# Performance work log

Hardware: AMD Instinct MI355X
Metric: run time of the kernel (lower is better)

Reference implementation:

```python
import jax, jax.numpy as jnp
import numpy as np

B, N, C = 8, 1024, 768
H = 12
D = C // H  # head_dim = 64
SCALE = D ** -0.5
EPS = 1e-5


def _layer_norm(x):
    # per-head LayerNorm over last dim, gamma=1, beta=0, biased variance
    mean = x.mean(-1, keepdims=True)
    var = ((x - mean) ** 2).mean(-1, keepdims=True)
    return (x - mean) / jnp.sqrt(var + EPS)


def setup_inputs() -> dict:
    key = jax.random.key(0)
    k1, k2, k3 = jax.random.split(key, 3)
    x = jax.random.normal(k1, (B, N, C), dtype=jnp.float32)
    qkv_weight = jax.random.normal(k2, (3 * C, C), dtype=jnp.float32) * (C ** -0.5)
    proj_weight = jax.random.normal(k3, (C, C), dtype=jnp.float32) * (C ** -0.5)
    return {"x": x, "qkv_weight": qkv_weight, "proj_weight": proj_weight}


def reference(x, qkv_weight, proj_weight):
    Bx, Nx, Cx = x.shape
    qkv = x @ qkv_weight.T                          # [B,N,3C]
    qkv = qkv.reshape(Bx, Nx, 3, H, D).transpose(2, 0, 3, 1, 4)  # [3,B,H,N,D]
    q, k, v = qkv[0], qkv[1], qkv[2]
    q = _layer_norm(q) * SCALE
    k = _layer_norm(k)
    attn = jnp.einsum('bhnd,bhmd->bhnm', q, k)      # [B,H,N,N]
    attn = jax.nn.softmax(attn, axis=-1)
    out = jnp.einsum('bhnm,bhmd->bhnd', attn, v)    # [B,H,N,D]
    out = out.transpose(0, 2, 1, 3).reshape(Bx, Nx, Cx)
    return out @ proj_weight.T
```

## Files before the change

kernel.cpp:

```cpp
#include <hip/hip_runtime.h>
#include <stdint.h>
#include <stddef.h>

#define HB 8
#define HN 1024
#define HC 768
#define HH 12
#define HD 64
#define ROWS (HB*HN)
#define BH (HB*HH)

using s16x4  = __attribute__((ext_vector_type(4))) short;
using bf16x8 = __attribute__((ext_vector_type(8))) short;
using f32x4  = __attribute__((ext_vector_type(4))) float;

__device__ __forceinline__ short f2bf(float f) {
  union { float f; uint32_t u; } c; c.f = f;
  uint32_t u = c.u;
  uint32_t r = (u + 0x7fffu + ((u >> 16) & 1u)) >> 16;
  return (short)r;
}
__device__ __forceinline__ float bf2f(short s) {
  union { uint32_t u; float f; } c; c.u = ((uint32_t)(uint16_t)s) << 16;
  return c.f;
}
__device__ __forceinline__ uint32_t pack_bf16_rne(float a, float b) {
  union { float f; uint32_t u; } ca, cb; ca.f = a; cb.f = b;
  uint32_t ra = ca.u + 0x7fffu + ((ca.u >> 16) & 1u);
  uint32_t rb = cb.u + 0x7fffu + ((cb.u >> 16) & 1u);
  return __builtin_amdgcn_perm(rb, ra, 0x07060302);
}
__device__ __forceinline__ float fast_exp2(float x) {
#if __has_builtin(__builtin_amdgcn_exp2f)
  return __builtin_amdgcn_exp2f(x);
#else
  return exp2f(x);
#endif
}
__device__ __forceinline__ f32x4 mfma16(bf16x8 a, bf16x8 b, f32x4 c) {
  return __builtin_amdgcn_mfma_f32_16x16x32_bf16(a, b, c, 0, 0, 0);
}
__device__ __forceinline__ void gll16(const void* g, void* l) {
  __builtin_amdgcn_global_load_lds((const __attribute__((address_space(1))) void*)g,
                                   (__attribute__((address_space(3))) void*)l,
                                   16, 0, 0);
}

__global__ void cvt3_kernel(const float* __restrict__ x,  short* __restrict__ xb,  int n0,
                            const float* __restrict__ wq, short* __restrict__ wqb, int n1,
                            const float* __restrict__ wp, short* __restrict__ wpb, int n2) {
  int i = blockIdx.x * 256 + threadIdx.x;
  const float* in; short* out;
  if (i < n0)            { in = x;  out = xb;  }
  else if (i < n0 + n1)  { i -= n0; in = wq; out = wqb; }
  else if (i < n0 + n1 + n2) { i -= n0 + n1; in = wp; out = wpb; }
  else return;
  float4 v = ((const float4*)in)[i];
  s16x4 o;
  o.x = f2bf(v.x); o.y = f2bf(v.y); o.z = f2bf(v.z); o.w = f2bf(v.w);
  ((s16x4*)out)[i] = o;
}

__device__ __forceinline__ void store_c(float* p, float v) { *p = v; }
__device__ __forceinline__ void store_c(short* p, float v) { *p = f2bf(v); }

__global__ __launch_bounds__(256) void gemm_qkv(const short* __restrict__ A,
                                                const short* __restrict__ Bw,
                                                short* __restrict__ Qb,
                                                short* __restrict__ Kb,
                                                short* __restrict__ vb) {
  const int K = HC;
  __shared__ short As[128*64];
  __shared__ short Bs[128*64];
  const int m0 = blockIdx.y * 128, n0 = blockIdx.x * 128;
  const int tid = threadIdx.x;
  const int lane = tid & 63, w = tid >> 6, quad = lane >> 4, lc = lane & 15;
  const int wr = w >> 1, wc = w & 1;
  f32x4 acc[4][4] = {};
  for (int kt = 0; kt < K; kt += 64) {
#pragma unroll
    for (int i = 0; i < 4; ++i) {
      const int chunk = i*256 + tid;
      const int r = chunk >> 3, cb = chunk & 7;
      const int cbs = cb ^ (r & 7);
      gll16(A  + (size_t)(m0 + r)*K + kt + cbs*8, (void*)(As + (size_t)chunk*8));
      gll16(Bw + (size_t)(n0 + r)*K + kt + cbs*8, (void*)(Bs + (size_t)chunk*8));
    }
    __syncthreads();
#pragma unroll
    for (int kk = 0; kk < 2; ++kk) {
      bf16x8 af[4], bfr[4];
      const int kb = kk*4 + quad;
#pragma unroll
      for (int mt = 0; mt < 4; ++mt)
        af[mt] = *(const bf16x8*)(As + (wr*64 + mt*16 + lc)*64 + (kb ^ (lc & 7))*8);
#pragma unroll
      for (int nt = 0; nt < 4; ++nt)
        bfr[nt] = *(const bf16x8*)(Bs + (wc*64 + nt*16 + lc)*64 + (kb ^ (lc & 7))*8);
#pragma unroll
      for (int mt = 0; mt < 4; ++mt)
#pragma unroll
        for (int nt = 0; nt < 4; ++nt)
          acc[mt][nt] = mfma16(af[mt], bfr[nt], acc[mt][nt]);
    }
    __syncthreads();
  }
  const int cg = n0 + wc*64;
  const int t = cg / HC;
  const int h = (cg % HC) / HD;
  const int b = m0 >> 10;
  const int bh = b*HH + h;
  if (t < 2) {
    short* outp = (t == 0) ? Qb : Kb;
    const float sc = (t == 0) ? 0.125f : 1.0f;
#pragma unroll
    for (int mt = 0; mt < 4; ++mt)
#pragma unroll
      for (int r = 0; r < 4; ++r) {
        float s1 = (acc[mt][0][r] + acc[mt][1][r]) + (acc[mt][2][r] + acc[mt][3][r]);
        float s2 = acc[mt][0][r]*acc[mt][0][r];
        s2 = __builtin_fmaf(acc[mt][1][r], acc[mt][1][r], s2);
        s2 = __builtin_fmaf(acc[mt][2][r], acc[mt][2][r], s2);
        s2 = __builtin_fmaf(acc[mt][3][r], acc[mt][3][r], s2);
#pragma unroll
        for (int off = 1; off < 16; off <<= 1) {
          s1 += __shfl_xor(s1, off);
          s2 += __shfl_xor(s2, off);
        }
        const float mean = s1 * (1.0f/64.0f);
        const float var  = s2 * (1.0f/64.0f) - mean*mean;
        const float inv  = rsqrtf(var + 1e-5f) * sc;
        const int n_in = (m0 & 1023) + wr*64 + mt*16 + quad*4 + r;
        short* rowp = outp + ((size_t)bh*HN + n_in)*HD;
#pragma unroll
        for (int nt = 0; nt < 4; ++nt)
          rowp[nt*16 + lc] = f2bf((acc[mt][nt][r] - mean) * inv);
      }
  } else {
#pragma unroll
    for (int mt = 0; mt < 4; ++mt)
#pragma unroll
      for (int nt = 0; nt < 4; ++nt)
#pragma unroll
        for (int r = 0; r < 4; ++r) {
          const int row = m0 + wr*64 + mt*16 + quad*4 + r;
          const int col = h*HD + nt*16 + lc;
          vb[(size_t)row*HC + col] = f2bf(acc[mt][nt][r]);
        }
  }
}

__global__ __launch_bounds__(256) void gemm_bt_f32(const short* __restrict__ A,
                                                   const short* __restrict__ Bw,
                                                   float* __restrict__ C,
                                                   int M, int N, int K) {
  __shared__ short As[128*64];
  __shared__ short Bs[128*64];
  const int m0 = blockIdx.y * 128, n0 = blockIdx.x * 128;
  const int tid = threadIdx.x;
  const int lane = tid & 63, w = tid >> 6, quad = lane >> 4, lc = lane & 15;
  const int wr = w >> 1, wc = w & 1;
  f32x4 acc[4][4] = {};
  for (int kt = 0; kt < K; kt += 64) {
#pragma unroll
    for (int i = 0; i < 4; ++i) {
      const int chunk = i*256 + tid;
      const int r = chunk >> 3, cb = chunk & 7;
      const int cbs = cb ^ (r & 7);
      gll16(A  + (size_t)(m0 + r)*K + kt + cbs*8, (void*)(As + (size_t)chunk*8));
      gll16(Bw + (size_t)(n0 + r)*K + kt + cbs*8, (void*)(Bs + (size_t)chunk*8));
    }
    __syncthreads();
#pragma unroll
    for (int kk = 0; kk < 2; ++kk) {
      bf16x8 af[4], bfr[4];
      const int kb = kk*4 + quad;
#pragma unroll
      for (int mt = 0; mt < 4; ++mt)
        af[mt] = *(const bf16x8*)(As + (wr*64 + mt*16 + lc)*64 + (kb ^ (lc & 7))*8);
#pragma unroll
      for (int nt = 0; nt < 4; ++nt)
        bfr[nt] = *(const bf16x8*)(Bs + (wc*64 + nt*16 + lc)*64 + (kb ^ (lc & 7))*8);
#pragma unroll
      for (int mt = 0; mt < 4; ++mt)
#pragma unroll
        for (int nt = 0; nt < 4; ++nt)
          acc[mt][nt] = mfma16(af[mt], bfr[nt], acc[mt][nt]);
    }
    __syncthreads();
  }
#pragma unroll
  for (int mt = 0; mt < 4; ++mt)
#pragma unroll
    for (int nt = 0; nt < 4; ++nt)
#pragma unroll
      for (int r = 0; r < 4; ++r) {
        const int row = m0 + wr*64 + mt*16 + quad*4 + r;
        const int col = n0 + wc*64 + nt*16 + lc;
        store_c(C + (size_t)row*N + col, acc[mt][nt][r]);
      }
}

__global__ __launch_bounds__(256) void vtrans_kernel(const short* __restrict__ vb,
                                                     short* __restrict__ Vtb) {
  const int blk = blockIdx.x;
  const int tile = blk & 7, bh = blk >> 3;
  const int b = bh / HH, h = bh % HH;
  const int n0 = tile * 128;
  const int tid = threadIdx.x;
  __shared__ float vt[128][65];
#pragma unroll
  for (int i = 0; i < 32; ++i) {
    const int idx = i*256 + tid; const int r = idx >> 6, dcol = idx & 63;
    vt[r][dcol] = bf2f(vb[(size_t)(b*HN + n0 + r)*HC + h*HD + dcol]);
  }
  __syncthreads();
#pragma unroll
  for (int it = 0; it < 4; ++it) {
    const int idx = it*256 + tid;
    const int dd = idx >> 4, j8 = idx & 15;
    bf16x8 o;
#pragma unroll
    for (int u = 0; u < 8; ++u) {
      const int c  = j8*8 + u;
      const int g  = c >> 6, cl = c & 63;
      const int k  = g*64 + ((cl & 3)*16 + (cl >> 2));
      o[u] = f2bf(vt[k][dd]);
    }
    *(bf16x8*)(Vtb + ((size_t)bh*HD + dd)*HN + n0 + j8*8) = o;
  }
}

__global__ __launch_bounds__(256, 4) void attn_kernel(const short* __restrict__ Qb,
                                                      const short* __restrict__ Kb,
                                                      const short* __restrict__ Vtb,
                                                      short* __restrict__ AOb) {
  const int blk = blockIdx.x;
  const int qt = blk & 15, bh = blk >> 4;
  const int b = bh / HH, h = bh % HH;
  const int tid = threadIdx.x, w = tid >> 6, lane = tid & 63;
  const int quad = lane >> 4, lc = lane & 15;

  __shared__ short Ks [64][72];
  __shared__ short Vts[64][72];
  __shared__ short Ps [4][16][72];

  const int mrow = qt*64 + w*16 + lc;
  bf16x8 aq[2];
  aq[0] = *(const bf16x8*)(Qb + ((size_t)bh*HN + mrow)*HD + quad*8);
  aq[1] = *(const bf16x8*)(Qb + ((size_t)bh*HN + mrow)*HD + 32 + quad*8);

  const short* kbh = Kb  + (size_t)bh*HN*HD;
  const short* vbh = Vtb + (size_t)bh*HD*HN;

  f32x4 oacc[4] = {};
  float l_i[4] = {0.f, 0.f, 0.f, 0.f};

  bf16x8 gk[2], gv[2];
#pragma unroll
  for (int i = 0; i < 2; ++i) {
    const int c = i*256 + tid;
    gk[i] = *(const bf16x8*)(kbh + (size_t)(c >> 3)*HD + (c & 7)*8);
    gv[i] = *(const bf16x8*)(vbh + (size_t)(c >> 3)*HN + (c & 7)*8);
  }
#pragma unroll
  for (int i = 0; i < 2; ++i) {
    const int c = i*256 + tid;
    *(bf16x8*)(&Ks [c >> 3][(c & 7)*8]) = gk[i];
    *(bf16x8*)(&Vts[c >> 3][(c & 7)*8]) = gv[i];
  }
  __syncthreads();

  const float LOG2E = 1.44269504f;
  const float MB2   = 8.0f * 1.44269504f;

  for (int ck = 0; ck < 16; ++ck) {
    if (ck < 15) {
      const int nn0 = (ck + 1)*64;
#pragma unroll
      for (int i = 0; i < 2; ++i) {
        const int c = i*256 + tid;
        gk[i] = *(const bf16x8*)(kbh + (size_t)(nn0 + (c >> 3))*HD + (c & 7)*8);
        gv[i] = *(const bf16x8*)(vbh + (size_t)(c >> 3)*HN + nn0 + (c & 7)*8);
      }
    }

    f32x4 sacc[4] = {};
#pragma unroll
    for (int kk = 0; kk < 2; ++kk)
#pragma unroll
      for (int nt = 0; nt < 4; ++nt) {
        bf16x8 bk = *(const bf16x8*)(&Ks[nt*16 + lc][kk*32 + quad*8]);
        sacc[nt] = mfma16(aq[kk], bk, sacc[nt]);
      }

#pragma unroll
    for (int r = 0; r < 4; ++r) {
      float ps[4];
#pragma unroll
      for (int nt = 0; nt < 4; ++nt) {
        ps[nt] = fast_exp2(__builtin_fmaf(sacc[nt][r], LOG2E, -MB2));
        sacc[nt][r] = ps[nt];
      }
      l_i[r] += (ps[0] + ps[1]) + (ps[2] + ps[3]);
    }

#pragma unroll
    for (int r = 0; r < 4; ++r) {
      uint2 pk;
      pk.x = pack_bf16_rne(sacc[0][r], sacc[1][r]);
      pk.y = pack_bf16_rne(sacc[2][r], sacc[3][r]);
      *(uint2*)(&Ps[w][quad*4 + r][lc*4]) = pk;
    }

#pragma unroll
    for (int kk = 0; kk < 2; ++kk) {
      bf16x8 ap = *(const bf16x8*)(&Ps[w][lc][kk*32 + quad*8]);
#pragma unroll
      for (int nt2 = 0; nt2 < 4; ++nt2) {
        bf16x8 bv = *(const bf16x8*)(&Vts[nt2*16 + lc][kk*32 + quad*8]);
        oacc[nt2] = mfma16(ap, bv, oacc[nt2]);
      }
    }

    if (ck < 15) {
      __syncthreads();
#pragma unroll
      for (int i = 0; i < 2; ++i) {
        const int c = i*256 + tid;
        *(bf16x8*)(&Ks [c >> 3][(c & 7)*8]) = gk[i];
        *(bf16x8*)(&Vts[c >> 3][(c & 7)*8]) = gv[i];
      }
      __syncthreads();
    }
  }

  float rl[4];
#pragma unroll
  for (int r = 0; r < 4; ++r) {
    float l = l_i[r];
#pragma unroll
    for (int off = 1; off < 16; off <<= 1) l += __shfl_xor(l, off);
    rl[r] = 1.0f / l;
  }
#pragma unroll
  for (int nt2 = 0; nt2 < 4; ++nt2)
#pragma unroll
    for (int r = 0; r < 4; ++r) {
      const int row = qt*64 + w*16 + quad*4 + r;
      const int d   = nt2*16 + lc;
      AOb[((size_t)(b*HN + row))*HC + h*HD + d] = f2bf(oacc[nt2][r] * rl[r]);
    }
}

extern "C" void kernel_launch(void* const* d_in, const int* in_sizes, int n_in,
                              void* d_out, int out_size, void* d_ws, size_t ws_size,
                              hipStream_t stream) {
  const float* x     = (const float*)d_in[0];
  const float* wqkv  = (const float*)d_in[1];
  const float* wproj = (const float*)d_in[2];
  float* out = (float*)d_out;

  char* ws = (char*)d_ws;
  size_t off = 0;
  auto alloc = [&](size_t bytes) -> void* {
    void* p = ws + off; off += (bytes + 255) & ~(size_t)255; return p;
  };
  short* xb     = (short*)alloc((size_t)ROWS*HC*2);
  short* wqkvb  = (short*)alloc((size_t)3*HC*HC*2);
  short* wprojb = (short*)alloc((size_t)HC*HC*2);
  short* vb     = (short*)alloc((size_t)ROWS*HC*2);
  short* Qb     = (short*)alloc((size_t)BH*HN*HD*2);
  short* Kb     = (short*)alloc((size_t)BH*HN*HD*2);
  short* Vtb    = (short*)alloc((size_t)BH*HD*HN*2);
  short* AOb    = (short*)alloc((size_t)ROWS*HC*2);

  { const int n0 = ROWS*HC/4, n1 = 3*HC*HC/4, n2 = HC*HC/4;
    const int tot = n0 + n1 + n2;
    cvt3_kernel<<<(tot + 255)/256, 256, 0, stream>>>(x, xb, n0, wqkv, wqkvb, n1,
                                                     wproj, wprojb, n2); }

  gemm_qkv<<<dim3(3*HC/128, ROWS/128), 256, 0, stream>>>(xb, wqkvb, Qb, Kb, vb);
  vtrans_kernel<<<BH*8, 256, 0, stream>>>(vb, Vtb);
  attn_kernel<<<BH*16, 256, 0, stream>>>(Qb, Kb, Vtb, AOb);
  gemm_bt_f32<<<dim3(HC/128, ROWS/128), 256, 0, stream>>>(AOb, wprojb, out,
                                                          ROWS, HC, HC);
}
```

Measured before the change: 208.5 us.

## Fuse V transpose into QKV GEMM epilogue and remap blocks per XCD

```diff
diff --git a/kernel.cpp b/kernel.cpp
--- a/kernel.cpp
+++ b/kernel.cpp
@@ -68,11 +68,15 @@
                                                 const short* __restrict__ Bw,
                                                 short* __restrict__ Qb,
                                                 short* __restrict__ Kb,
-                                                short* __restrict__ vb) {
+                                                short* __restrict__ Vtb) {
   const int K = HC;
-  __shared__ short As[128*64];
-  __shared__ short Bs[128*64];
-  const int m0 = blockIdx.y * 128, n0 = blockIdx.x * 128;
+  __shared__ short sm[2*128*64];
+  short* As = sm;
+  short* Bs = sm + 128*64;
+  const int bid = blockIdx.x;
+  const int xcd = bid & 7, lin = bid >> 3;
+  const int bx = lin % 18, by = xcd*8 + lin/18;
+  const int m0 = by * 128, n0 = bx * 128;
   const int tid = threadIdx.x;
   const int lane = tid & 63, w = tid >> 6, quad = lane >> 4, lc = lane & 15;
   const int wr = w >> 1, wc = w & 1;
@@ -105,12 +109,12 @@
     }
     __syncthreads();
   }
-  const int cg = n0 + wc*64;
-  const int t = cg / HC;
-  const int h = (cg % HC) / HD;
   const int b = m0 >> 10;
-  const int bh = b*HH + h;
-  if (t < 2) {
+  if (bx < 12) {
+    const int cg = n0 + wc*64;
+    const int t = cg / HC;
+    const int h = (cg % HC) / HD;
+    const int bh = b*HH + h;
     short* outp = (t == 0) ? Qb : Kb;
     const float sc = (t == 0) ? 0.125f : 1.0f;
 #pragma unroll
@@ -137,16 +141,37 @@
           rowp[nt*16 + lc] = f2bf((acc[mt][nt][r] - mean) * inv);
       }
   } else {
-#pragma unroll
-    for (int mt = 0; mt < 4; ++mt)
-#pragma unroll
-      for (int nt = 0; nt < 4; ++nt)
-#pragma unroll
-        for (int r = 0; r < 4; ++r) {
-          const int row = m0 + wr*64 + mt*16 + quad*4 + r;
-          const int col = h*HD + nt*16 + lc;
-          vb[(size_t)row*HC + col] = f2bf(acc[mt][nt][r]);
+    short (*Tt)[132] = (short(*)[132])sm;
+    const int h0 = (bx - 12) * 2;
+    const int nb = m0 & 1023;
+#pragma unroll
+    for (int p = 0; p < 2; ++p) {
+      if (wr == p) {
+#pragma unroll
+        for (int mt = 0; mt < 4; ++mt)
+#pragma unroll
+          for (int nt = 0; nt < 4; ++nt)
+#pragma unroll
+            for (int r = 0; r < 4; ++r)
+              Tt[mt*16 + quad*4 + r][wc*64 + nt*16 + lc] = f2bf(acc[mt][nt][r]);
+      }
+      __syncthreads();
+#pragma unroll
+      for (int it = 0; it < 4; ++it) {
+        const int id = it*256 + tid;
+        const int dd = id >> 3, j = id & 7;
+        bf16x8 o;
+#pragma unroll
+        for (int u = 0; u < 8; ++u) {
+          const int c = j*8 + u;
+          const int k = (c & 3)*16 + (c >> 2);
+          o[u] = Tt[k][dd];
         }
+        const int bhv = b*HH + h0 + (dd >> 6);
+        *(bf16x8*)(Vtb + ((size_t)bhv*HD + (dd & 63))*HN + nb + p*64 + j*8) = o;
+      }
+      __syncthreads();
+    }
   }
 }
 
@@ -156,7 +181,10 @@
                                                    int M, int N, int K) {
   __shared__ short As[128*64];
   __shared__ short Bs[128*64];
-  const int m0 = blockIdx.y * 128, n0 = blockIdx.x * 128;
+  const int bid = blockIdx.x;
+  const int xcd = bid & 7, lin = bid >> 3;
+  const int bx = lin % 6, by = xcd*8 + lin/6;
+  const int m0 = by * 128, n0 = bx * 128;
   const int tid = threadIdx.x;
   const int lane = tid & 63, w = tid >> 6, quad = lane >> 4, lc = lane & 15;
   const int wr = w >> 1, wc = w & 1;
@@ -201,42 +229,13 @@
       }
 }
 
-__global__ __launch_bounds__(256) void vtrans_kernel(const short* __restrict__ vb,
-                                                     short* __restrict__ Vtb) {
-  const int blk = blockIdx.x;
-  const int tile = blk & 7, bh = blk >> 3;
-  const int b = bh / HH, h = bh % HH;
-  const int n0 = tile * 128;
-  const int tid = threadIdx.x;
-  __shared__ float vt[128][65];
-#pragma unroll
-  for (int i = 0; i < 32; ++i) {
-    const int idx = i*256 + tid; const int r = idx >> 6, dcol = idx & 63;
-    vt[r][dcol] = bf2f(vb[(size_t)(b*HN + n0 + r)*HC + h*HD + dcol]);
-  }
-  __syncthreads();
-#pragma unroll
-  for (int it = 0; it < 4; ++it) {
-    const int idx = it*256 + tid;
-    const int dd = idx >> 4, j8 = idx & 15;
-    bf16x8 o;
-#pragma unroll
-    for (int u = 0; u < 8; ++u) {
-      const int c  = j8*8 + u;
-      const int g  = c >> 6, cl = c & 63;
-      const int k  = g*64 + ((cl & 3)*16 + (cl >> 2));
-      o[u] = f2bf(vt[k][dd]);
-    }
-    *(bf16x8*)(Vtb + ((size_t)bh*HD + dd)*HN + n0 + j8*8) = o;
-  }
-}
-
 __global__ __launch_bounds__(256, 4) void attn_kernel(const short* __restrict__ Qb,
                                                       const short* __restrict__ Kb,
                                                       const short* __restrict__ Vtb,
                                                       short* __restrict__ AOb) {
   const int blk = blockIdx.x;
-  const int qt = blk & 15, bh = blk >> 4;
+  const int xcd = blk & 7, lin = blk >> 3;
+  const int bh = xcd*12 + lin % 12, qt = lin / 12;
   const int b = bh / HH, h = bh % HH;
   const int tid = threadIdx.x, w = tid >> 6, lane = tid & 63;
   const int quad = lane >> 4, lc = lane & 15;
@@ -369,7 +368,6 @@
   short* xb     = (short*)alloc((size_t)ROWS*HC*2);
   short* wqkvb  = (short*)alloc((size_t)3*HC*HC*2);
   short* wprojb = (short*)alloc((size_t)HC*HC*2);
-  short* vb     = (short*)alloc((size_t)ROWS*HC*2);
   short* Qb     = (short*)alloc((size_t)BH*HN*HD*2);
   short* Kb     = (short*)alloc((size_t)BH*HN*HD*2);
   short* Vtb    = (short*)alloc((size_t)BH*HD*HN*2);
@@ -380,9 +378,7 @@
     cvt3_kernel<<<(tot + 255)/256, 256, 0, stream>>>(x, xb, n0, wqkv, wqkvb, n1,
                                                      wproj, wprojb, n2); }
 
-  gemm_qkv<<<dim3(3*HC/128, ROWS/128), 256, 0, stream>>>(xb, wqkvb, Qb, Kb, vb);
-  vtrans_kernel<<<BH*8, 256, 0, stream>>>(vb, Vtb);
+  gemm_qkv<<<18*64, 256, 0, stream>>>(xb, wqkvb, Qb, Kb, Vtb);
   attn_kernel<<<BH*16, 256, 0, stream>>>(Qb, Kb, Vtb, AOb);
-  gemm_bt_f32<<<dim3(HC/128, ROWS/128), 256, 0, stream>>>(AOb, wprojb, out,
-                                                          ROWS, HC, HC);
-}
+  gemm_bt_f32<<<6*64, 256, 0, stream>>>(AOb, wprojb, out, ROWS, HC, HC);
+}
```

Result: slower. 229.5 us (+10.0%).

## Double query rows per attention block to reuse K/V tiles across two M-tiles

Applied to the files above, without the earlier changes.

```diff
diff --git a/kernel.cpp b/kernel.cpp
--- a/kernel.cpp
+++ b/kernel.cpp
@@ -231,30 +231,33 @@
   }
 }
 
-__global__ __launch_bounds__(256, 4) void attn_kernel(const short* __restrict__ Qb,
+__global__ __launch_bounds__(256, 3) void attn_kernel(const short* __restrict__ Qb,
                                                       const short* __restrict__ Kb,
                                                       const short* __restrict__ Vtb,
                                                       short* __restrict__ AOb) {
   const int blk = blockIdx.x;
-  const int qt = blk & 15, bh = blk >> 4;
+  const int qt = blk & 7, bh = blk >> 3;
   const int b = bh / HH, h = bh % HH;
   const int tid = threadIdx.x, w = tid >> 6, lane = tid & 63;
   const int quad = lane >> 4, lc = lane & 15;
 
   __shared__ short Ks [64][72];
   __shared__ short Vts[64][72];
-  __shared__ short Ps [4][16][72];
-
-  const int mrow = qt*64 + w*16 + lc;
-  bf16x8 aq[2];
-  aq[0] = *(const bf16x8*)(Qb + ((size_t)bh*HN + mrow)*HD + quad*8);
-  aq[1] = *(const bf16x8*)(Qb + ((size_t)bh*HN + mrow)*HD + 32 + quad*8);
+  __shared__ short Ps [4][32][72];
+
+  bf16x8 aq[2][2];
+#pragma unroll
+  for (int mt = 0; mt < 2; ++mt) {
+    const int mrow = qt*128 + w*32 + mt*16 + lc;
+    aq[mt][0] = *(const bf16x8*)(Qb + ((size_t)bh*HN + mrow)*HD + quad*8);
+    aq[mt][1] = *(const bf16x8*)(Qb + ((size_t)bh*HN + mrow)*HD + 32 + quad*8);
+  }
 
   const short* kbh = Kb  + (size_t)bh*HN*HD;
   const short* vbh = Vtb + (size_t)bh*HD*HN;
 
-  f32x4 oacc[4] = {};
-  float l_i[4] = {0.f, 0.f, 0.f, 0.f};
+  f32x4 oacc[2][4] = {};
+  float l_i[2][4] = {};
 
   bf16x8 gk[2], gv[2];
 #pragma unroll
@@ -285,41 +288,46 @@
       }
     }
 
-    f32x4 sacc[4] = {};
+    f32x4 sacc[2][4] = {};
 #pragma unroll
     for (int kk = 0; kk < 2; ++kk)
 #pragma unroll
       for (int nt = 0; nt < 4; ++nt) {
         bf16x8 bk = *(const bf16x8*)(&Ks[nt*16 + lc][kk*32 + quad*8]);
-        sacc[nt] = mfma16(aq[kk], bk, sacc[nt]);
-      }
-
-#pragma unroll
-    for (int r = 0; r < 4; ++r) {
-      float ps[4];
-#pragma unroll
-      for (int nt = 0; nt < 4; ++nt) {
-        ps[nt] = fast_exp2(__builtin_fmaf(sacc[nt][r], LOG2E, -MB2));
-        sacc[nt][r] = ps[nt];
-      }
-      l_i[r] += (ps[0] + ps[1]) + (ps[2] + ps[3]);
-    }
-
-#pragma unroll
-    for (int r = 0; r < 4; ++r) {
-      uint2 pk;
-      pk.x = pack_bf16_rne(sacc[0][r], sacc[1][r]);
-      pk.y = pack_bf16_rne(sacc[2][r], sacc[3][r]);
-      *(uint2*)(&Ps[w][quad*4 + r][lc*4]) = pk;
-    }
+#pragma unroll
+        for (int mt = 0; mt < 2; ++mt)
+          sacc[mt][nt] = mfma16(aq[mt][kk], bk, sacc[mt][nt]);
+      }
+
+#pragma unroll
+    for (int mt = 0; mt < 2; ++mt)
+#pragma unroll
+      for (int r = 0; r < 4; ++r) {
+        float ps[4];
+#pragma unroll
+        for (int nt = 0; nt < 4; ++nt) {
+          ps[nt] = fast_exp2(__builtin_fmaf(sacc[mt][nt][r], LOG2E, -MB2));
+          sacc[mt][nt][r] = ps[nt];
+        }
+        l_i[mt][r] += (ps[0] + ps[1]) + (ps[2] + ps[3]);
+        uint2 pk;
+        pk.x = pack_bf16_rne(ps[0], ps[1]);
+        pk.y = pack_bf16_rne(ps[2], ps[3]);
+        *(uint2*)(&Ps[w][mt*16 + quad*4 + r][lc*4]) = pk;
+      }
 
 #pragma unroll
     for (int kk = 0; kk < 2; ++kk) {
-      bf16x8 ap = *(const bf16x8*)(&Ps[w][lc][kk*32 + quad*8]);
+      bf16x8 ap[2];
+#pragma unroll
+      for (int mt = 0; mt < 2; ++mt)
+        ap[mt] = *(const bf16x8*)(&Ps[w][mt*16 + lc][kk*32 + quad*8]);
 #pragma unroll
       for (int nt2 = 0; nt2 < 4; ++nt2) {
         bf16x8 bv = *(const bf16x8*)(&Vts[nt2*16 + lc][kk*32 + quad*8]);
-        oacc[nt2] = mfma16(ap, bv, oacc[nt2]);
+#pragma unroll
+        for (int mt = 0; mt < 2; ++mt)
+          oacc[mt][nt2] = mfma16(ap[mt], bv, oacc[mt][nt2]);
       }
     }
 
@@ -335,21 +343,20 @@
     }
   }
 
-  float rl[4];
-#pragma unroll
-  for (int r = 0; r < 4; ++r) {
-    float l = l_i[r];
-#pragma unroll
-    for (int off = 1; off < 16; off <<= 1) l += __shfl_xor(l, off);
-    rl[r] = 1.0f / l;
-  }
-#pragma unroll
-  for (int nt2 = 0; nt2 < 4; ++nt2)
+#pragma unroll
+  for (int mt = 0; mt < 2; ++mt)
 #pragma unroll
     for (int r = 0; r < 4; ++r) {
-      const int row = qt*64 + w*16 + quad*4 + r;
-      const int d   = nt2*16 + lc;
-      AOb[((size_t)(b*HN + row))*HC + h*HD + d] = f2bf(oacc[nt2][r] * rl[r]);
+      float l = l_i[mt][r];
+#pragma unroll
+      for (int off = 1; off < 16; off <<= 1) l += __shfl_xor(l, off);
+      const float rl = 1.0f / l;
+      const int row = qt*128 + w*32 + mt*16 + quad*4 + r;
+#pragma unroll
+      for (int nt2 = 0; nt2 < 4; ++nt2) {
+        const int d = nt2*16 + lc;
+        AOb[((size_t)(b*HN + row))*HC + h*HD + d] = f2bf(oacc[mt][nt2][r] * rl);
+      }
     }
 }
 
@@ -382,7 +389,7 @@
 
   gemm_qkv<<<dim3(3*HC/128, ROWS/128), 256, 0, stream>>>(xb, wqkvb, Qb, Kb, vb);
   vtrans_kernel<<<BH*8, 256, 0, stream>>>(vb, Vtb);
-  attn_kernel<<<BH*16, 256, 0, stream>>>(Qb, Kb, Vtb, AOb);
+  attn_kernel<<<BH*8, 256, 0, stream>>>(Qb, Kb, Vtb, AOb);
   gemm_bt_f32<<<dim3(HC/128, ROWS/128), 256, 0, stream>>>(AOb, wprojb, out,
                                                           ROWS, HC, HC);
 }
```

After: 203.2 us. 2.6% less time.
